# Optimization experiments

Measured on AMD Instinct MI355X. Metric: run time of the kernel, lower is better.

The kernel has to match this reference:

```python
import jax, jax.numpy as jnp
import numpy as np

N_NODES = 100000
N_EDGES = 3200000
F_IN = 128
F_OUT = 32
N_GRAPHS = 64


def setup_inputs() -> dict:
    key = jax.random.key(0)
    ks = jax.random.split(key, 12)
    x = jax.random.normal(ks[0], (N_NODES, F_IN), dtype=jnp.float32)
    edge_attr = jax.random.normal(ks[1], (N_EDGES, 1), dtype=jnp.float32)
    edge_index = jax.random.randint(ks[2], (2, N_EDGES), 0, N_NODES, dtype=jnp.int64)
    batch = jnp.sort(jax.random.randint(ks[3], (N_NODES,), 0, N_GRAPHS, dtype=jnp.int64))
    s = 1.0 / np.sqrt(F_IN)
    W_l = jax.random.normal(ks[4], (F_IN, F_OUT), dtype=jnp.float32) * s
    b_l = jnp.zeros((F_OUT,), dtype=jnp.float32)
    W_r = jax.random.normal(ks[5], (F_IN, F_OUT), dtype=jnp.float32) * s
    b_r = jnp.zeros((F_OUT,), dtype=jnp.float32)
    W_e = jax.random.normal(ks[6], (1, F_OUT), dtype=jnp.float32)
    att = jax.random.normal(ks[7], (F_OUT,), dtype=jnp.float32) * (1.0 / np.sqrt(F_OUT))
    bias = jnp.zeros((F_OUT,), dtype=jnp.float32)
    return {"x": x, "edge_attr": edge_attr, "W_l": W_l, "b_l": b_l,
            "W_r": W_r, "b_r": b_r, "W_e": W_e, "att": att, "bias": bias,
            "edge_index": edge_index, "batch": batch}


def reference(x, edge_attr, W_l, b_l, W_r, b_r, W_e, att, bias, edge_index, batch):
    # GATv2Conv (heads=1, concat=True, edge_dim=1, negative_slope=0.2)
    src = edge_index[0]  # message source j
    dst = edge_index[1]  # message target i
    xl = x @ W_l + b_l            # [N, F_OUT] source transform
    xr = x @ W_r + b_r            # [N, F_OUT] target transform
    e = edge_attr @ W_e           # [E, F_OUT] edge feature embedding
    m = xl[src] + xr[dst] + e     # [E, F_OUT]
    m = jax.nn.leaky_relu(m, negative_slope=0.2)
    logit = m @ att               # [E] per-edge attention logit
    # segment softmax over incoming edges of each target node
    mx = jax.ops.segment_max(logit, dst, num_segments=N_NODES)
    alpha = jnp.exp(logit - mx[dst])
    denom = jax.ops.segment_sum(alpha, dst, num_segments=N_NODES)
    alpha = alpha / (denom[dst] + 1e-16)
    # weighted scatter aggregation of source messages, then output bias
    out = jax.ops.segment_sum(xl[src] * alpha[:, None], dst, num_segments=N_NODES) + bias
    # global_mean_pool over graphs
    cnt = jax.ops.segment_sum(jnp.ones((N_NODES,), x.dtype), batch, num_segments=N_GRAPHS)
    pooled = jax.ops.segment_sum(out, batch, num_segments=N_GRAPHS) / jnp.maximum(cnt, 1.0)[:, None]
    return pooled  # [N_GRAPHS, F_OUT]
```

## Files before the change

kernel.cpp:

```cpp
#include <hip/hip_runtime.h>
#include <hip/hip_fp16.h>

#define N_NODES 100000
#define N_EDGES 3200000
#define F_IN 128
#define F_OUT 32
#define N_GRAPHS 64

#define UNROLL 4

#define DPP_QUAD_XOR1   0xB1
#define DPP_QUAD_XOR2   0x4E
#define DPP_HALF_MIRROR 0x141
#define DPP_ROW_MIRROR  0x140

template <int CTRL>
__device__ __forceinline__ float dpp_add(float v) {
    return v + __int_as_float(__builtin_amdgcn_update_dpp(
        0, __float_as_int(v), CTRL, 0xF, 0xF, true));
}

__global__ __launch_bounds__(256) void gat_transform(
    const float* __restrict__ x,
    const float* __restrict__ Wl, const float* __restrict__ bl,
    const float* __restrict__ Wr, const float* __restrict__ br,
    __half* __restrict__ xl16, __half* __restrict__ xr16)
{
    __shared__ float2 sW[F_IN * F_OUT];
    for (int i = threadIdx.x; i < F_IN * F_OUT; i += 256)
        sW[i] = make_float2(Wl[i], Wr[i]);
    __syncthreads();

    const int f     = threadIdx.x & 31;
    const int node0 = blockIdx.x * 32 + (threadIdx.x >> 5) * 4;

    const float4* x0 = (const float4*)(x + (size_t)(node0 + 0) * F_IN);
    const float4* x1 = (const float4*)(x + (size_t)(node0 + 1) * F_IN);
    const float4* x2 = (const float4*)(x + (size_t)(node0 + 2) * F_IN);
    const float4* x3 = (const float4*)(x + (size_t)(node0 + 3) * F_IN);

    const float bl_f = bl[f], br_f = br[f];
    float a0 = bl_f, a1 = bl_f, a2 = bl_f, a3 = bl_f;
    float r0 = br_f, r1 = br_f, r2 = br_f, r3 = br_f;

#pragma unroll 4
    for (int k4 = 0; k4 < F_IN / 4; ++k4) {
        float4 v0 = x0[k4], v1 = x1[k4], v2 = x2[k4], v3 = x3[k4];
        float2 w0 = sW[(4 * k4 + 0) * 32 + f];
        float2 w1 = sW[(4 * k4 + 1) * 32 + f];
        float2 w2 = sW[(4 * k4 + 2) * 32 + f];
        float2 w3 = sW[(4 * k4 + 3) * 32 + f];
        a0 += v0.x * w0.x + v0.y * w1.x + v0.z * w2.x + v0.w * w3.x;
        r0 += v0.x * w0.y + v0.y * w1.y + v0.z * w2.y + v0.w * w3.y;
        a1 += v1.x * w0.x + v1.y * w1.x + v1.z * w2.x + v1.w * w3.x;
        r1 += v1.x * w0.y + v1.y * w1.y + v1.z * w2.y + v1.w * w3.y;
        a2 += v2.x * w0.x + v2.y * w1.x + v2.z * w2.x + v2.w * w3.x;
        r2 += v2.x * w0.y + v2.y * w1.y + v2.z * w2.y + v2.w * w3.y;
        a3 += v3.x * w0.x + v3.y * w1.x + v3.z * w2.x + v3.w * w3.x;
        r3 += v3.x * w0.y + v3.y * w1.y + v3.z * w2.y + v3.w * w3.y;
    }
    xl16[(size_t)(node0 + 0) * 32 + f] = __float2half_rn(a0);
    xl16[(size_t)(node0 + 1) * 32 + f] = __float2half_rn(a1);
    xl16[(size_t)(node0 + 2) * 32 + f] = __float2half_rn(a2);
    xl16[(size_t)(node0 + 3) * 32 + f] = __float2half_rn(a3);
    xr16[(size_t)(node0 + 0) * 32 + f] = __float2half_rn(r0);
    xr16[(size_t)(node0 + 1) * 32 + f] = __float2half_rn(r1);
    xr16[(size_t)(node0 + 2) * 32 + f] = __float2half_rn(r2);
    xr16[(size_t)(node0 + 3) * 32 + f] = __float2half_rn(r3);
}

__global__ __launch_bounds__(256) void gat_edge16(
    const int* __restrict__ ei, const float* __restrict__ eattr,
    const float* __restrict__ We, const float* __restrict__ att,
    const __half* __restrict__ xl16, const __half* __restrict__ xr16,
    float* __restrict__ outacc, float* __restrict__ denom)
{
    const int f = threadIdx.x & 31;
    const float attf = att[f];
    const float wef  = We[f];
    const int group = (blockIdx.x * blockDim.x + threadIdx.x) >> 5;
    const int ng    = (gridDim.x * blockDim.x) >> 5;

    for (int e0 = group; e0 < N_EDGES; e0 += UNROLL * ng) {
        int  eIdx[UNROLL];
        bool val[UNROLL];
        int  src[UNROLL], dst[UNROLL];
        float ea[UNROLL], xlv[UNROLL], xrv[UNROLL];

#pragma unroll
        for (int u = 0; u < UNROLL; ++u) {
            const int e = e0 + u * ng;
            val[u]  = (e < N_EDGES);
            eIdx[u] = val[u] ? e : e0;
        }
#pragma unroll
        for (int u = 0; u < UNROLL; ++u) {
            src[u] = ei[eIdx[u]];
            dst[u] = ei[N_EDGES + eIdx[u]];
            ea[u]  = eattr[eIdx[u]];
        }
#pragma unroll
        for (int u = 0; u < UNROLL; ++u) {
            xlv[u] = __half2float(xl16[(size_t)src[u] * 32 + f]);
            xrv[u] = __half2float(xr16[(size_t)dst[u] * 32 + f]);
        }
#pragma unroll
        for (int u = 0; u < UNROLL; ++u) {
            float m = xlv[u] + xrv[u] + ea[u] * wef;
            m = (m > 0.f) ? m : 0.2f * m;
            float t = m * attf;
            t = dpp_add<DPP_QUAD_XOR1>(t);
            t = dpp_add<DPP_QUAD_XOR2>(t);
            t = dpp_add<DPP_HALF_MIRROR>(t);
            t = dpp_add<DPP_ROW_MIRROR>(t);
            t += __shfl_xor(t, 16, 32);
            const float p = __expf(t);
            if (val[u]) {
                unsafeAtomicAdd(&outacc[(size_t)dst[u] * 32 + f], xlv[u] * p);
                if (f == 0) unsafeAtomicAdd(&denom[dst[u]], p);
            }
        }
    }
}

__global__ __launch_bounds__(256) void gat_pool_div(
    const float* __restrict__ outacc, const float* __restrict__ denom,
    const float* __restrict__ bias, const int* __restrict__ batch,
    float* __restrict__ out)
{
    const int g = blockIdx.x;
    __shared__ int s_lo, s_hi;
    if (threadIdx.x == 0) {
        int lo = 0, hi = N_NODES;
        while (lo < hi) { int mid = (lo + hi) >> 1; if (batch[mid] < g) lo = mid + 1; else hi = mid; }
        s_lo = lo;
        lo = 0; hi = N_NODES;
        while (lo < hi) { int mid = (lo + hi) >> 1; if (batch[mid] < g + 1) lo = mid + 1; else hi = mid; }
        s_hi = lo;
    }
    __syncthreads();
    const int lo = s_lo, hi = s_hi;

    const int f   = threadIdx.x & 31;
    const int grp = threadIdx.x >> 5;

    float acc = 0.f;
    for (int n = lo + grp; n < hi; n += 8)
        acc += outacc[(size_t)n * 32 + f] / (denom[n] + 1e-16f);

    __shared__ float s_acc[8][32];
    s_acc[grp][f] = acc;
    __syncthreads();

    if (threadIdx.x < 32) {
        float sum = 0.f;
#pragma unroll
        for (int i = 0; i < 8; ++i) sum += s_acc[i][f];
        const int cnt = hi - lo;
        out[g * 32 + f] = (cnt > 0) ? (sum / (float)cnt + bias[f]) : 0.f;
    }
}

extern "C" void kernel_launch(void* const* d_in, const int* in_sizes, int n_in,
                              void* d_out, int out_size, void* d_ws, size_t ws_size,
                              hipStream_t stream)
{
    const float* x     = (const float*)d_in[0];
    const float* eattr = (const float*)d_in[1];
    const float* Wl    = (const float*)d_in[2];
    const float* bl    = (const float*)d_in[3];
    const float* Wr    = (const float*)d_in[4];
    const float* br    = (const float*)d_in[5];
    const float* We    = (const float*)d_in[6];
    const float* att   = (const float*)d_in[7];
    const float* bias  = (const float*)d_in[8];
    const int*   ei    = (const int*)d_in[9];
    const int*   batch = (const int*)d_in[10];
    float* out = (float*)d_out;

    const size_t NF = (size_t)N_NODES * 32;

    __half* xl16   = (__half*)d_ws;
    __half* xr16   = xl16 + NF;
    float*  outacc = (float*)(xr16 + NF);
    float*  denom  = outacc + NF;

    hipMemsetAsync(outacc, 0, (NF + N_NODES) * sizeof(float), stream);

    gat_transform<<<N_NODES / 32, 256, 0, stream>>>(x, Wl, bl, Wr, br, xl16, xr16);
    gat_edge16<<<4096, 256, 0, stream>>>(ei, eattr, We, att, xl16, xr16, outacc, denom);
    gat_pool_div<<<N_GRAPHS, 256, 0, stream>>>(outacc, denom, bias, batch, out);
}
```

Before: 635.8 us.

## Partition edges into src/dst node-range buckets for cache-local gathers and atomics

Adds a histogram, scan and scatter pass that bins edges into 64 buckets by source and destination node partition, packing local indices and the edge attribute into one 8-byte record. The edge kernel then walks each bucket so that xl/xr gathers and outacc atomics touch a limited node range, aiming for better L2 locality. This costs three extra kernels, including a single-block scan, plus an extra read and write of the edge list every call.

```diff
diff --git a/kernel.cpp b/kernel.cpp
--- a/kernel.cpp
+++ b/kernel.cpp
@@ -7,6 +7,12 @@
 #define F_OUT 32
 #define N_GRAPHS 64
 
+#define NP   8
+#define PSZ  (N_NODES / NP)
+#define NBKT 64
+#define NCH  256
+#define CHUNK (N_EDGES / NCH)
+#define NREG (NBKT * NCH)
 #define UNROLL 4
 
 #define DPP_QUAD_XOR1   0xB1
@@ -69,44 +75,116 @@
     xr16[(size_t)(node0 + 3) * 32 + f] = __float2half_rn(r3);
 }
 
-__global__ __launch_bounds__(256) void gat_edge16(
-    const int* __restrict__ ei, const float* __restrict__ eattr,
+__global__ __launch_bounds__(256) void part_hist(const int* __restrict__ ei,
+                                                 int* __restrict__ cnt)
+{
+    __shared__ int h[NBKT];
+    if (threadIdx.x < NBKT) h[threadIdx.x] = 0;
+    __syncthreads();
+    const int c  = blockIdx.x;
+    const int e0 = c * CHUNK;
+    for (int i = threadIdx.x; i < CHUNK; i += 256) {
+        const int src = __builtin_nontemporal_load(&ei[e0 + i]);
+        const int dst = __builtin_nontemporal_load(&ei[N_EDGES + e0 + i]);
+        atomicAdd(&h[src / PSZ + NP * (dst / PSZ)], 1);
+    }
+    __syncthreads();
+    if (threadIdx.x < NBKT) cnt[threadIdx.x * NCH + c] = h[threadIdx.x];
+}
+
+__global__ __launch_bounds__(1024) void part_scan(const int* __restrict__ cnt,
+                                                  int* __restrict__ base)
+{
+    __shared__ int s[1024];
+    const int t = threadIdx.x;
+    int loc[16];
+    int sum = 0;
+#pragma unroll
+    for (int r = 0; r < 16; ++r) { loc[r] = cnt[t * 16 + r]; sum += loc[r]; }
+    s[t] = sum;
+    __syncthreads();
+    for (int off = 1; off < 1024; off <<= 1) {
+        const int u = (t >= off) ? s[t - off] : 0;
+        __syncthreads();
+        s[t] += u;
+        __syncthreads();
+    }
+    int run = s[t] - sum;
+#pragma unroll
+    for (int r = 0; r < 16; ++r) { base[t * 16 + r] = run; run += loc[r]; }
+    if (t == 1023) base[NREG] = run;
+}
+
+__global__ __launch_bounds__(256) void part_scatter(const int* __restrict__ ei,
+                                                    const float* __restrict__ eattr,
+                                                    const int* __restrict__ base,
+                                                    int2* __restrict__ es2)
+{
+    __shared__ int cur[NBKT];
+    const int c = blockIdx.x;
+    if (threadIdx.x < NBKT) cur[threadIdx.x] = base[threadIdx.x * NCH + c];
+    __syncthreads();
+    const int e0 = c * CHUNK;
+    for (int i = threadIdx.x; i < CHUNK; i += 256) {
+        const int src = __builtin_nontemporal_load(&ei[e0 + i]);
+        const int dst = __builtin_nontemporal_load(&ei[N_EDGES + e0 + i]);
+        const float ea = __builtin_nontemporal_load(&eattr[e0 + i]);
+        const int sp = src / PSZ, dp = dst / PSZ;
+        const int srcl = src - sp * PSZ;
+        const int dstl = dst - dp * PSZ;
+        const int pos = atomicAdd(&cur[sp + NP * dp], 1);
+        const long long raw = (long long)(unsigned)(srcl | (dstl << 14))
+                            | ((long long)__float_as_int(ea) << 32);
+        __builtin_nontemporal_store(raw, (long long*)&es2[pos]);
+    }
+}
+
+__global__ __launch_bounds__(256) void gat_edge_part(
+    const int2* __restrict__ es2, const int* __restrict__ base,
     const float* __restrict__ We, const float* __restrict__ att,
     const __half* __restrict__ xl16, const __half* __restrict__ xr16,
     float* __restrict__ outacc, float* __restrict__ denom)
 {
+    const int b    = blockIdx.x;
+    const int bkt  = b & (NBKT - 1);
+    const int slot = b >> 6;
+    const int srcb = (bkt & (NP - 1)) * PSZ;
+    const int dstb = (bkt >> 3) * PSZ;
+
+    const int beg = base[bkt * NCH + slot * 8];
+    const int end = base[bkt * NCH + slot * 8 + 8];
+
     const int f = threadIdx.x & 31;
+    const int g = threadIdx.x >> 5;
     const float attf = att[f];
     const float wef  = We[f];
-    const int group = (blockIdx.x * blockDim.x + threadIdx.x) >> 5;
-    const int ng    = (gridDim.x * blockDim.x) >> 5;
-
-    for (int e0 = group; e0 < N_EDGES; e0 += UNROLL * ng) {
-        int  eIdx[UNROLL];
+
+    const long long* es8 = (const long long*)es2;
+
+    for (int e0 = beg + g; e0 < end; e0 += 8 * UNROLL) {
+        long long raw[UNROLL];
         bool val[UNROLL];
-        int  src[UNROLL], dst[UNROLL];
-        float ea[UNROLL], xlv[UNROLL], xrv[UNROLL];
+        float xlv[UNROLL], xrv[UNROLL];
+        int   dst[UNROLL];
 
 #pragma unroll
         for (int u = 0; u < UNROLL; ++u) {
-            const int e = e0 + u * ng;
-            val[u]  = (e < N_EDGES);
-            eIdx[u] = val[u] ? e : e0;
+            const int j = e0 + u * 8;
+            val[u] = (j < end);
+            raw[u] = __builtin_nontemporal_load(&es8[val[u] ? j : beg]);
         }
 #pragma unroll
         for (int u = 0; u < UNROLL; ++u) {
-            src[u] = ei[eIdx[u]];
-            dst[u] = ei[N_EDGES + eIdx[u]];
-            ea[u]  = eattr[eIdx[u]];
-        }
-#pragma unroll
-        for (int u = 0; u < UNROLL; ++u) {
-            xlv[u] = __half2float(xl16[(size_t)src[u] * 32 + f]);
+            const int lo   = (int)raw[u];
+            const int src  = srcb + (lo & 0x3FFF);
+            dst[u]         = dstb + ((lo >> 14) & 0x3FFF);
+            xlv[u] = __half2float(xl16[(size_t)src * 32 + f]);
             xrv[u] = __half2float(xr16[(size_t)dst[u] * 32 + f]);
         }
 #pragma unroll
         for (int u = 0; u < UNROLL; ++u) {
-            float m = xlv[u] + xrv[u] + ea[u] * wef;
+            const float ea = __int_as_float((int)(raw[u] >> 32));
+            float m = xlv[u] + xrv[u] + ea * wef;
             m = (m > 0.f) ? m : 0.2f * m;
             float t = m * attf;
             t = dpp_add<DPP_QUAD_XOR1>(t);
@@ -184,10 +262,16 @@
     __half* xr16   = xl16 + NF;
     float*  outacc = (float*)(xr16 + NF);
     float*  denom  = outacc + NF;
+    int2*   es2    = (int2*)(denom + N_NODES);
+    int*    cnt    = (int*)(es2 + N_EDGES);
+    int*    base   = cnt + NREG;
 
     hipMemsetAsync(outacc, 0, (NF + N_NODES) * sizeof(float), stream);
 
     gat_transform<<<N_NODES / 32, 256, 0, stream>>>(x, Wl, bl, Wr, br, xl16, xr16);
-    gat_edge16<<<4096, 256, 0, stream>>>(ei, eattr, We, att, xl16, xr16, outacc, denom);
+    part_hist<<<NCH, 256, 0, stream>>>(ei, cnt);
+    part_scan<<<1, 1024, 0, stream>>>(cnt, base);
+    part_scatter<<<NCH, 256, 0, stream>>>(ei, eattr, base, es2);
+    gat_edge_part<<<2048, 256, 0, stream>>>(es2, base, We, att, xl16, xr16, outacc, denom);
     gat_pool_div<<<N_GRAPHS, 256, 0, stream>>>(outacc, denom, bias, batch, out);
 }
```

Result: slower. 735.0 us (+15.6%).
